# Performance work log

Hardware: AMD Instinct MI355X
Metric: run time of the kernel (lower is better)

The kernel has to match this reference:

```python
import jax, jax.numpy as jnp
import numpy as np

N = 10000      # nodes
E = 100000     # edges
D = 768        # hidden = heads * head_dim
H = 4          # heads
C = D // H     # 192 per-head channels
EDIM = 16      # edge feature dim
NREL = 10      # num relations
L = 3          # num TransformerConv layers


def setup_inputs() -> dict:
    key = jax.random.key(0)
    ks = jax.random.split(key, 16)
    s = 0.02
    x = jax.random.normal(ks[0], (N, D), jnp.float32)
    edge_index = jax.random.randint(ks[1], (2, E), 0, N, jnp.int32)
    rel = jax.random.randint(ks[2], (E,), 0, NREL).astype(jnp.float32)
    w = jax.random.uniform(ks[3], (E,), jnp.float32)
    edge_attr = jnp.stack([rel, w], axis=1)  # [E, 2]: (relation_id, weight)
    rel_emb = jax.random.normal(ks[4], (NREL, EDIM - 1), jnp.float32) * s
    W_edge = jax.random.normal(ks[5], (EDIM, EDIM), jnp.float32) * s
    b_edge = jnp.zeros((EDIM,), jnp.float32)
    Wk = jax.random.normal(ks[6], (L, D, D), jnp.float32) * s
    bk = jnp.zeros((L, D), jnp.float32)
    Wq = jax.random.normal(ks[7], (L, D, D), jnp.float32) * s
    bq = jnp.zeros((L, D), jnp.float32)
    Wv = jax.random.normal(ks[8], (L, D, D), jnp.float32) * s
    bv = jnp.zeros((L, D), jnp.float32)
    We = jax.random.normal(ks[9], (L, EDIM, D), jnp.float32) * s   # lin_edge, no bias (PyG)
    Wskip = jax.random.normal(ks[10], (L, D, D), jnp.float32) * s  # root/skip linear
    bskip = jnp.zeros((L, D), jnp.float32)
    ln_g = jnp.ones((D,), jnp.float32)
    ln_b = jnp.zeros((D,), jnp.float32)
    return dict(x=x, edge_attr=edge_attr, edge_index=edge_index, rel_emb=rel_emb,
                W_edge=W_edge, b_edge=b_edge, Wk=Wk, bk=bk, Wq=Wq, bq=bq,
                Wv=Wv, bv=bv, We=We, Wskip=Wskip, bskip=bskip, ln_g=ln_g, ln_b=ln_b)


def reference(x, edge_attr, edge_index, rel_emb, W_edge, b_edge,
              Wk, bk, Wq, bq, Wv, bv, We, Wskip, bskip, ln_g, ln_b):
    src, dst = edge_index[0], edge_index[1]
    # _process_edge_features: embed relation id, concat weight, project
    rel_ids = jnp.clip(jax.lax.stop_gradient(edge_attr[:, 0]).astype(jnp.int32), 0, NREL - 1)
    ef = jnp.concatenate([rel_emb[rel_ids], edge_attr[:, 1:2]], axis=-1) @ W_edge + b_edge  # [E,16]
    scale = 1.0 / np.sqrt(C)
    h = x  # input_proj is Identity (input_dim == hidden_dim)
    for l in range(L):
        q = (h @ Wq[l] + bq[l]).reshape(N, H, C)
        k = (h @ Wk[l] + bk[l]).reshape(N, H, C)
        v = (h @ Wv[l] + bv[l]).reshape(N, H, C)
        e = (ef @ We[l]).reshape(E, H, C)           # per-edge embedding
        kj = k[src] + e                              # [E,H,C]
        alpha = jnp.einsum('ehc,ehc->eh', q[dst], kj) * scale  # [E,H]
        # scatter-softmax over incoming edges of each destination node
        m = jax.ops.segment_max(jax.lax.stop_gradient(alpha), dst, num_segments=N)
        a = jnp.exp(alpha - m[dst])
        denom = jax.ops.segment_sum(a, dst, num_segments=N)
        a = a / (denom[dst] + 1e-16)
        msg = (v[src] + e) * a[..., None]            # [E,H,C]
        out = jax.ops.segment_sum(msg.reshape(E, H * C), dst, num_segments=N)
        h = out + h @ Wskip[l] + bskip[l]            # root_weight skip connection
        if l < L - 1:
            h = jax.nn.gelu(h, approximate=False)    # dropout: eval mode -> identity
    mu = jnp.mean(h, axis=-1, keepdims=True)
    var = jnp.mean((h - mu) ** 2, axis=-1, keepdims=True)
    h = (h - mu) / jnp.sqrt(var + 1e-5) * ln_g + ln_b
    return jnp.mean(h, axis=0)  # global_mean_pool over single graph -> [D]
```

## Files before the change

kernel.cpp:

```cpp
#include <hip/hip_runtime.h>
#include <hip/hip_bf16.h>
#include <math.h>
#include <stdint.h>

#define NN 10000
#define EE 100000
#define DD 768
#define HH 4
#define CC 192
#define EDIM 16
#define NREL 10
#define MP 10240
#define NQ2 3200
#define NB 3136
#define SCALE 0.07216878364870322f

using short8  = __attribute__((ext_vector_type(8))) short;
using floatx4 = __attribute__((ext_vector_type(4))) float;


__device__ __forceinline__ float b2f(short u) {
    union { unsigned int i; float f; } t;
    t.i = ((unsigned int)(unsigned short)u) << 16;
    return t.f;
}

__device__ __forceinline__ short f2b(float f) {
    __hip_bfloat16 h = __float2bfloat16(f);
    short r;
    __builtin_memcpy(&r, &h, 2);
    return r;
}

__device__ __forceinline__ __hip_bfloat16 rd_any(const void* p, long long j, int bf) {
    if (bf) return ((const __hip_bfloat16*)p)[j];
    return __float2bfloat16(((const float*)p)[j]);
}

__device__ __forceinline__ void gload16(const __hip_bfloat16* g, __hip_bfloat16* l) {
    __builtin_amdgcn_global_load_lds(
        (const __attribute__((address_space(1))) unsigned int*)g,
        (__attribute__((address_space(3))) unsigned int*)l, 16, 0, 0);
}

__global__ __launch_bounds__(256) void detect_zero(const void* edge_attr,
                                                   int* flag, int* counts) {
    int i = blockIdx.x * 256 + threadIdx.x;
    if (i < NN) counts[i] = 0;
    if (blockIdx.x == 0 && threadIdx.x < 64) {
        const unsigned short* p = (const unsigned short*)edge_attr;
        int nz = (p[4 * threadIdx.x] != 0) ? 1 : 0;
        unsigned long long m = __ballot(nz);
        if (threadIdx.x == 0) *flag = (__popcll(m) > 8) ? 1 : 0;
    }
}


__global__ __launch_bounds__(256) void cvt_big(
    const void* x, const void* We, const int* flag,
    __hip_bfloat16* hb, __hip_bfloat16* Web) {
    long long i = (long long)blockIdx.x * 256 + threadIdx.x;
    int bf = *flag;
    const long long NX = (long long)NN * DD;
    const long long NE2 = 3LL * EDIM * DD;
    if (i < NX) { hb[i] = rd_any(x, i, bf); return; } i -= NX;
    if (i < NE2) { Web[i] = rd_any(We, i, bf); return; } i -= NE2;
    if (i < (long long)(MP - NN) * DD) hb[(long long)NN * DD + i] = __float2bfloat16(0.0f);
}

__global__ __launch_bounds__(256) void cvt_small(
    const void* ea, const void* rel, const void* Wed, const void* bed,
    const void* bk, const void* bq, const void* bv, const void* bs,
    const void* lg, const void* lb, const int* flag,
    __hip_bfloat16* eab, __hip_bfloat16* relb, __hip_bfloat16* Wedb,
    __hip_bfloat16* bedb, __hip_bfloat16* ballb, __hip_bfloat16* lgb,
    __hip_bfloat16* lbb) {
    long long i = (long long)blockIdx.x * 256 + threadIdx.x;
    int bf = *flag;
    if (i < 2LL * EE) { eab[i] = rd_any(ea, i, bf); return; } i -= 2LL * EE;
    if (i < NREL * (EDIM - 1)) { relb[i] = rd_any(rel, i, bf); return; } i -= NREL * (EDIM - 1);
    if (i < EDIM * EDIM) { Wedb[i] = rd_any(Wed, i, bf); return; } i -= EDIM * EDIM;
    if (i < EDIM) { bedb[i] = rd_any(bed, i, bf); return; } i -= EDIM;
    if (i < 3 * NB) {
        int l = (int)(i / NB), c = (int)(i % NB);
        const void* src; long long off;
        if (c < 768)       { src = bq; off = (long long)l * DD + c; }
        else if (c < 1536) { src = bk; off = (long long)l * DD + (c - 768); }
        else if (c < 2304) { src = bv; off = (long long)l * DD + (c - 1536); }
        else if (c < 3072) { src = bs; off = (long long)l * DD + (c - 2304); }
        else { ballb[i] = __float2bfloat16(0.0f); return; }
        ballb[i] = rd_any(src, off, bf); return;
    } i -= 3 * NB;
    if (i < DD) { lgb[i] = rd_any(lg, i, bf); return; } i -= DD;
    if (i < DD) { lbb[i] = rd_any(lb, i, bf); return; }
}

__global__ __launch_bounds__(256) void wt_all(
    const void* Wq, const void* Wk, const void* Wv, const void* Ws,
    const int* flag, __hip_bfloat16* Wt3) {
    __shared__ __hip_bfloat16 tile[32][33];
    int mm = blockIdx.y;
    int l = mm >> 2, m = mm & 3;
    const void* src = (m == 0) ? Wq : (m == 1) ? Wk : (m == 2) ? Wv : Ws;
    int bx = blockIdx.x;
    int tr = bx / 24, tc = bx % 24;
    int k0 = tr * 32, c0 = tc * 32;
    int t = threadIdx.x;
    int rr = t >> 5, cc = t & 31;
    int bf = *flag;
    long long base = (long long)l * DD * DD;
#pragma unroll
    for (int p = 0; p < 4; p++)
        tile[p * 8 + rr][cc] =
            rd_any(src, base + (long long)(k0 + p * 8 + rr) * DD + c0 + cc, bf);
    __syncthreads();
    __hip_bfloat16* dst = Wt3 + (size_t)l * NB * DD + (size_t)(m * 768 + c0) * DD + k0;
#pragma unroll
    for (int p = 0; p < 4; p++)
        dst[(size_t)(p * 8 + rr) * DD + cc] = tile[cc][p * 8 + rr];
}

__global__ __launch_bounds__(256) void mq_kernel(
    const void* Wq, const void* bq, const int* flag,
    const __hip_bfloat16* __restrict__ Web, __hip_bfloat16* __restrict__ Wt3,
    __hip_bfloat16* __restrict__ ballb) {
    __shared__ float WeS[16][193];
    const int lh = blockIdx.y, l = lh >> 2, hh = lh & 3;
    const int t = threadIdx.x;
    const int bf = *flag;
    for (int i = t; i < 16 * 192; i += 256) {
        int j = i / 192, c = i % 192;
        WeS[j][c] = (float)Web[(size_t)l * EDIM * DD + (size_t)j * DD + hh * CC + c];
    }
    __syncthreads();
    const int k = blockIdx.x * 64 + (t >> 2);
    const int j0 = (t & 3) * 4;
    float s0 = 0.f, s1 = 0.f, s2 = 0.f, s3 = 0.f;
    if (bf) {
        const short8* qp = (const short8*)((const __hip_bfloat16*)Wq +
            ((size_t)l * DD + k) * DD + hh * CC);
#pragma unroll 4
        for (int ch = 0; ch < 24; ch++) {
            short8 v = qp[ch];
#pragma unroll
            for (int u = 0; u < 8; u++) {
                float w = b2f(v[u]);
                int c = ch * 8 + u;
                s0 += w * WeS[j0 + 0][c]; s1 += w * WeS[j0 + 1][c];
                s2 += w * WeS[j0 + 2][c]; s3 += w * WeS[j0 + 3][c];
            }
        }
    } else {
        const float4* qp = (const float4*)((const float*)Wq +
            ((size_t)l * DD + k) * DD + hh * CC);
#pragma unroll 4
        for (int ch = 0; ch < 48; ch++) {
            float4 v = qp[ch];
            float wv[4] = {v.x, v.y, v.z, v.w};
#pragma unroll
            for (int u = 0; u < 4; u++) {
                float w = wv[u];
                int c = ch * 4 + u;
                s0 += w * WeS[j0 + 0][c]; s1 += w * WeS[j0 + 1][c];
                s2 += w * WeS[j0 + 2][c]; s3 += w * WeS[j0 + 3][c];
            }
        }
    }
    const size_t base = (size_t)l * NB * DD;
    const int row = 3072 + hh * 16 + j0;
    Wt3[base + (size_t)(row + 0) * DD + k] = __float2bfloat16(s0);
    Wt3[base + (size_t)(row + 1) * DD + k] = __float2bfloat16(s1);
    Wt3[base + (size_t)(row + 2) * DD + k] = __float2bfloat16(s2);
    Wt3[base + (size_t)(row + 3) * DD + k] = __float2bfloat16(s3);
    if (blockIdx.x == 0 && t < 4) {
        float b0 = 0.f, b1 = 0.f, b2 = 0.f, b3 = 0.f;
        for (int c = 0; c < CC; c++) {
            float w = (float)rd_any(bq, (long long)l * DD + hh * CC + c, bf);
            b0 += w * WeS[j0 + 0][c]; b1 += w * WeS[j0 + 1][c];
            b2 += w * WeS[j0 + 2][c]; b3 += w * WeS[j0 + 3][c];
        }
        ballb[l * NB + 3072 + hh * 16 + j0 + 0] = __float2bfloat16(b0);
        ballb[l * NB + 3072 + hh * 16 + j0 + 1] = __float2bfloat16(b1);
        ballb[l * NB + 3072 + hh * 16 + j0 + 2] = __float2bfloat16(b2);
        ballb[l * NB + 3072 + hh * 16 + j0 + 3] = __float2bfloat16(b3);
    }
}


__global__ __launch_bounds__(256) void count_kernel(const int* ei, int* counts) {
    int e = blockIdx.x * 256 + threadIdx.x;
    if (e < EE) atomicAdd(&counts[ei[EE + e]], 1);
}

__global__ __launch_bounds__(256) void scan_kernel(const int* counts, int* rowptr,
                                                   int* cursor) {
    __shared__ int sdata[256];
    int t = threadIdx.x;
    int base = t * 40;
    int cnt = (base < NN) ? min(40, NN - base) : 0;
    int s = 0;
    for (int i = 0; i < cnt; i++) s += counts[base + i];
    sdata[t] = s;
    __syncthreads();
    for (int off = 1; off < 256; off <<= 1) {
        int add = (t >= off) ? sdata[t - off] : 0;
        __syncthreads();
        sdata[t] += add;
        __syncthreads();
    }
    int run = sdata[t] - s;
    for (int i = 0; i < cnt; i++) {
        cursor[base + i] = run;
        run += counts[base + i];
        rowptr[base + i + 1] = run;
    }
    if (t == 0) rowptr[0] = 0;
}

__global__ __launch_bounds__(256) void fill_kernel(const int* ei, int* cursor,
                                                   int* eids, int* esrc) {
    int e = blockIdx.x * 256 + threadIdx.x;
    if (e < EE) {
        int d = ei[EE + e];
        int pos = atomicAdd(&cursor[d], 1);
        eids[pos] = e;
        esrc[pos] = ei[e];
    }
}


__global__ __launch_bounds__(256) void ef_kernel(
    const int* __restrict__ eids,
    const __hip_bfloat16* __restrict__ eab, const __hip_bfloat16* __restrict__ relb,
    const __hip_bfloat16* __restrict__ Wedb, const __hip_bfloat16* __restrict__ bedb,
    __hip_bfloat16* __restrict__ efb) {
    int idx = blockIdx.x * 256 + threadIdx.x;
    if (idx >= EE * EDIM) return;
    int p = idx >> 4, j = idx & 15;
    int e = eids[p];
    int rid = (int)((float)eab[e * 2 + 0]);
    rid = min(max(rid, 0), NREL - 1);
    float w = (float)eab[e * 2 + 1];
    float s = (float)bedb[j];
#pragma unroll
    for (int i = 0; i < 15; i++)
        s += (float)relb[rid * 15 + i] * (float)Wedb[i * EDIM + j];
    s += w * (float)Wedb[15 * EDIM + j];
    efb[idx] = __float2bfloat16(s);
}


__device__ __forceinline__ void stage_half(const __hip_bfloat16* g, int row0, int ktile,
                                           char* ldsdst, int tid) {
#pragma unroll
    for (int j = 0; j < 2; ++j) {
        int c = j * 512 + tid;
        int row = c >> 3;
        int sch = (c & 7) ^ (row & 7);
        gload16(g + (size_t)(row0 + row) * DD + ktile * 64 + sch * 8,
                (__hip_bfloat16*)(ldsdst + c * 16));
    }
}

#define MF16(va, vb, cc) cc = __builtin_amdgcn_mfma_f32_16x16x32_bf16(va, vb, cc, 0, 0, 0)
#define BAR() __builtin_amdgcn_s_barrier()
#define WLG() asm volatile("s_waitcnt lgkmcnt(0)" ::: "memory")
#define WVM(N) asm volatile("s_waitcnt vmcnt(" #N ")" ::: "memory")
#define SB() __builtin_amdgcn_sched_barrier(0)
#define LDS8(off) (*(const short8*)(smem + (off)))

__global__ __launch_bounds__(512) void gemm256(
    const __hip_bfloat16* __restrict__ A, const __hip_bfloat16* __restrict__ Bt,
    const __hip_bfloat16* __restrict__ bias, __hip_bfloat16* __restrict__ C) {
    __shared__ __align__(16) char smem[131072];
    const int bid = (int)blockIdx.x;
    const int tid = threadIdx.x;
    const int wid = tid >> 6, lane = tid & 63;
    const int quad = lane >> 4, l15 = lane & 15;

    if (bid >= 480) {
        const int qb = bid - 480;
        const int m0q = qb * 64;
        const __hip_bfloat16* Bq = Bt + (size_t)3072 * DD;
        const int xq0 = (quad ^ (l15 & 7)) * 16;
        const int xq1 = ((quad + 4) ^ (l15 & 7)) * 16;
        floatx4 qacc[4] = {};
        for (int kt = 0; kt < 12; ++kt) {
#pragma unroll
            for (int j = 0; j < 2; ++j) {
                int c = j * 512 + tid;
                int hf = c >> 9;
                int cc = c & 511;
                int row = cc >> 3;
                int sch = (cc & 7) ^ (row & 7);
                const __hip_bfloat16* src = hf
                    ? (Bq + (size_t)row * DD + kt * 64 + sch * 8)
                    : (A + (size_t)(m0q + row) * DD + kt * 64 + sch * 8);
                gload16(src, (__hip_bfloat16*)(smem + c * 16));
            }
            asm volatile("s_waitcnt vmcnt(0)" ::: "memory");
            BAR();
            if (wid < 4) {
                short8 a0 = LDS8((wid * 16 + l15) * 128 + xq0);
                short8 a1 = LDS8((wid * 16 + l15) * 128 + xq1);
#pragma unroll
                for (int nt = 0; nt < 4; ++nt) {
                    short8 b0 = LDS8(8192 + (nt * 16 + l15) * 128 + xq0);
                    short8 b1 = LDS8(8192 + (nt * 16 + l15) * 128 + xq1);
                    MF16(a0, b0, qacc[nt]);
                    MF16(a1, b1, qacc[nt]);
                }
            }
            WLG();
            BAR();
        }
        if (wid < 4) {
#pragma unroll
            for (int nt = 0; nt < 4; ++nt) {
                float bb = (float)bias[3072 + nt * 16 + l15];
#pragma unroll
                for (int r = 0; r < 4; ++r) {
                    int row = m0q + wid * 16 + quad * 4 + r;
                    if (row < NN)
                        C[(size_t)row * NQ2 + 3072 + nt * 16 + l15] =
                            __float2bfloat16(qacc[nt][r] + bb);
                }
            }
        }
        return;
    }

    const int wm = wid >> 2, wn = wid & 3;
    const int swz = (bid & 7) * 60 + (bid >> 3);
    const int m0 = (swz / 12) * 256;
    const int n0 = (swz % 12) * 256;

    const int xa0 = (quad ^ (l15 & 7)) * 16;
    const int xa1 = ((quad + 4) ^ (l15 & 7)) * 16;
    const int aRow = (wm * 128 + l15) * 128;
    const int bRow = 32768 + (wn * 64 + l15) * 128;

    floatx4 acc[8][4] = {};
    short8 a[4][2], bA[2][2], bB[2][2];

    stage_half(A, m0, 0, smem + 0, tid);
    stage_half(A, m0 + 128, 0, smem + 16384, tid);
    stage_half(Bt, n0, 0, smem + 32768, tid);
    stage_half(Bt, n0 + 128, 0, smem + 49152, tid);
    stage_half(Bt, n0, 1, smem + 98304, tid);
    stage_half(Bt, n0 + 128, 1, smem + 114688, tid);
    WVM(4);
    BAR();

#pragma unroll 1
    for (int it = 0; it < 6; ++it) {
        const int kA = 2 * it + 1;
        const int kB = (it < 5) ? 2 * it + 2 : 0;
        const int kC = (it < 5) ? 2 * it + 3 : 1;
        stage_half(A, m0, kA, smem + 65536, tid);
        stage_half(A, m0 + 128, kA, smem + 81920, tid);
#pragma unroll
        for (int mt = 0; mt < 4; ++mt) {
            a[mt][0] = LDS8(aRow + mt * 2048 + xa0);
            a[mt][1] = LDS8(aRow + mt * 2048 + xa1);
        }
#pragma unroll
        for (int nt = 0; nt < 2; ++nt) {
            bA[nt][0] = LDS8(bRow + nt * 2048 + xa0);
            bA[nt][1] = LDS8(bRow + nt * 2048 + xa1);
            bB[nt][0] = LDS8(bRow + (nt + 2) * 2048 + xa0);
            bB[nt][1] = LDS8(bRow + (nt + 2) * 2048 + xa1);
        }
        SB(); BAR(); WLG(); SB();
        __builtin_amdgcn_s_setprio(1);
#pragma unroll
        for (int mt = 0; mt < 4; ++mt)
#pragma unroll
            for (int nt = 0; nt < 2; ++nt) {
                MF16(a[mt][0], bA[nt][0], acc[mt][nt]);
                MF16(a[mt][1], bA[nt][1], acc[mt][nt]);
                MF16(a[mt][0], bB[nt][0], acc[mt][nt + 2]);
                MF16(a[mt][1], bB[nt][1], acc[mt][nt + 2]);
            }
        __builtin_amdgcn_s_setprio(0);
        stage_half(Bt, n0, kB, smem + 32768, tid);
        stage_half(Bt, n0 + 128, kB, smem + 49152, tid);
#pragma unroll
        for (int mt = 0; mt < 4; ++mt) {
            a[mt][0] = LDS8(aRow + (mt + 4) * 2048 + xa0);
            a[mt][1] = LDS8(aRow + (mt + 4) * 2048 + xa1);
        }
        WVM(4);
        SB(); BAR(); WLG(); SB();
        __builtin_amdgcn_s_setprio(1);
#pragma unroll
        for (int mt = 0; mt < 4; ++mt)
#pragma unroll
            for (int nt = 0; nt < 2; ++nt) {
                MF16(a[mt][0], bB[nt][0], acc[mt + 4][nt + 2]);
                MF16(a[mt][1], bB[nt][1], acc[mt + 4][nt + 2]);
                MF16(a[mt][0], bA[nt][0], acc[mt + 4][nt]);
                MF16(a[mt][1], bA[nt][1], acc[mt + 4][nt]);
            }
        __builtin_amdgcn_s_setprio(0);
        stage_half(A, m0, kB, smem + 0, tid);
        stage_half(A, m0 + 128, kB, smem + 16384, tid);
#pragma unroll
        for (int mt = 0; mt < 4; ++mt) {
            a[mt][0] = LDS8(65536 + aRow + mt * 2048 + xa0);
            a[mt][1] = LDS8(65536 + aRow + mt * 2048 + xa1);
        }
#pragma unroll
        for (int nt = 0; nt < 2; ++nt) {
            bA[nt][0] = LDS8(65536 + bRow + nt * 2048 + xa0);
            bA[nt][1] = LDS8(65536 + bRow + nt * 2048 + xa1);
            bB[nt][0] = LDS8(65536 + bRow + (nt + 2) * 2048 + xa0);
            bB[nt][1] = LDS8(65536 + bRow + (nt + 2) * 2048 + xa1);
        }
        SB(); BAR(); WLG(); SB();
        __builtin_amdgcn_s_setprio(1);
#pragma unroll
        for (int mt = 0; mt < 4; ++mt)
#pragma unroll
            for (int nt = 0; nt < 2; ++nt) {
                MF16(a[mt][0], bA[nt][0], acc[mt][nt]);
                MF16(a[mt][1], bA[nt][1], acc[mt][nt]);
                MF16(a[mt][0], bB[nt][0], acc[mt][nt + 2]);
                MF16(a[mt][1], bB[nt][1], acc[mt][nt + 2]);
            }
        __builtin_amdgcn_s_setprio(0);
        stage_half(Bt, n0, kC, smem + 98304, tid);
        stage_half(Bt, n0 + 128, kC, smem + 114688, tid);
#pragma unroll
        for (int mt = 0; mt < 4; ++mt) {
            a[mt][0] = LDS8(65536 + aRow + (mt + 4) * 2048 + xa0);
            a[mt][1] = LDS8(65536 + aRow + (mt + 4) * 2048 + xa1);
        }
        WVM(4);
        SB(); BAR(); WLG(); SB();
        __builtin_amdgcn_s_setprio(1);
#pragma unroll
        for (int mt = 0; mt < 4; ++mt)
#pragma unroll
            for (int nt = 0; nt < 2; ++nt) {
                MF16(a[mt][0], bB[nt][0], acc[mt + 4][nt + 2]);
                MF16(a[mt][1], bB[nt][1], acc[mt + 4][nt + 2]);
                MF16(a[mt][0], bA[nt][0], acc[mt + 4][nt]);
                MF16(a[mt][1], bA[nt][1], acc[mt + 4][nt]);
            }
        __builtin_amdgcn_s_setprio(0);
    }

    asm volatile("s_waitcnt vmcnt(0)" ::: "memory");
    BAR();
    {
        short* stg = (short*)smem + wid * 1152;
        float bv[4];
#pragma unroll
        for (int nt = 0; nt < 4; ++nt)
            bv[nt] = (float)bias[n0 + wn * 64 + nt * 16 + l15];
        const int rdo = (lane >> 2) * 68 + (lane & 3) * 16;
        const int grow0 = m0 + wm * 128 + (lane >> 2);
        const int gcol = n0 + wn * 64 + (lane & 3) * 16;
#pragma unroll
        for (int mt = 0; mt < 8; ++mt) {
#pragma unroll
            for (int nt = 0; nt < 4; ++nt)
#pragma unroll
                for (int r = 0; r < 4; ++r)
                    stg[(quad * 4 + r) * 68 + nt * 16 + l15] =
                        f2b(acc[mt][nt][r] + bv[nt]);
            asm volatile("s_waitcnt lgkmcnt(0)" ::: "memory");
            short8 v0 = *(const short8*)(stg + rdo);
            short8 v1 = *(const short8*)(stg + rdo + 8);
            int grow = grow0 + mt * 16;
            if (grow < NN) {
                short8* dp = (short8*)(C + (size_t)grow * NQ2 + gcol);
                dp[0] = v0; dp[1] = v1;
            }
            asm volatile("s_waitcnt lgkmcnt(0)" ::: "memory");
        }
    }
}


__global__ __launch_bounds__(256) void node_attn(
    const int* __restrict__ rowptr, const int* __restrict__ esrc,
    const __hip_bfloat16* __restrict__ qkvs, const __hip_bfloat16* __restrict__ efb,
    const __hip_bfloat16* __restrict__ Wel, __hip_bfloat16* __restrict__ hb,
    int do_gelu) {
    const int wv = threadIdx.x >> 6, lane = threadIdx.x & 63;
    const int n = blockIdx.x * 2 + (wv >> 1);
    const int half = wv & 1;
    const int cb = half * 384 + lane * 6;
    const int sj = lane & 15;
    const int hsel = lane & 32;
    const float qe_gate = ((lane & 16) == 0) ? 1.0f : 0.0f;
    const int s0 = rowptr[n], s1 = rowptr[n + 1];
    const short* qk = (const short*)qkvs;
    float q[6];
    {
        const short2* qp = (const short2*)(qk + (size_t)n * NQ2 + cb);
        short2 a = qp[0], b = qp[1], c = qp[2];
        q[0] = b2f(a.x) * SCALE; q[1] = b2f(a.y) * SCALE; q[2] = b2f(b.x) * SCALE;
        q[3] = b2f(b.y) * SCALE; q[4] = b2f(c.x) * SCALE; q[5] = b2f(c.y) * SCALE;
    }
    const float qe_l = b2f(qk[(size_t)n * NQ2 + 3072 + (half * 2 + (lane >> 5)) * 16 + sj])
                       * SCALE * qe_gate;
    float m = -INFINITY, lsum = 0.f, sacc = 0.f;
    float acc[6] = {};
    short2 ka = {0,0}, kb = {0,0}, kc = {0,0};
    short2 va = {0,0}, vb = {0,0}, vc = {0,0};
    float efv = 0.f;
    if (s0 < s1) {
        int src = esrc[s0];
        const short2* kp = (const short2*)(qk + (size_t)src * NQ2 + 768 + cb);
        const short2* vp = (const short2*)(qk + (size_t)src * NQ2 + 1536 + cb);
        ka = kp[0]; kb = kp[1]; kc = kp[2];
        va = vp[0]; vb = vp[1]; vc = vp[2];
        efv = b2f(((const short*)efb)[(size_t)s0 * 16 + sj]);
    }
    for (int p = s0; p < s1; p++) {
        short2 nka = ka, nkb = kb, nkc = kc, nva = va, nvb = vb, nvc = vc;
        float nefv = efv;
        if (p + 1 < s1) {
            int src = esrc[p + 1];
            const short2* kp = (const short2*)(qk + (size_t)src * NQ2 + 768 + cb);
            const short2* vp = (const short2*)(qk + (size_t)src * NQ2 + 1536 + cb);
            nka = kp[0]; nkb = kp[1]; nkc = kp[2];
            nva = vp[0]; nvb = vp[1]; nvc = vp[2];
            nefv = b2f(((const short*)efb)[(size_t)(p + 1) * 16 + sj]);
        }
        float part = qe_l * efv;
        part += q[0] * b2f(ka.x) + q[1] * b2f(ka.y) + q[2] * b2f(kb.x);
        part += q[3] * b2f(kb.y) + q[4] * b2f(kc.x) + q[5] * b2f(kc.y);
        part += __shfl_xor(part, 1); part += __shfl_xor(part, 2);
        part += __shfl_xor(part, 4); part += __shfl_xor(part, 8);
        part += __shfl_xor(part, 16);
        if (part > m + 8.0f) {
            float sc = __expf(m - part);
            m = part;
            lsum *= sc; sacc *= sc;
#pragma unroll
            for (int i = 0; i < 6; i++) acc[i] *= sc;
        }
        float w = __expf(part - m);
        lsum += w;
        sacc += w * efv;
        acc[0] += w * b2f(va.x); acc[1] += w * b2f(va.y);
        acc[2] += w * b2f(vb.x); acc[3] += w * b2f(vb.y);
        acc[4] += w * b2f(vc.x); acc[5] += w * b2f(vc.y);
        ka = nka; kb = nkb; kc = nkc; va = nva; vb = nvb; vc = nvc; efv = nefv;
    }
    float inv = 1.0f / (lsum + 1e-16f);
#pragma unroll
    for (int i = 0; i < 6; i++) acc[i] *= inv;
    float sS = sacc * inv;
    {
        const short2* sp = (const short2*)(qk + (size_t)n * NQ2 + 2304 + cb);
        short2 a = sp[0], b = sp[1], c = sp[2];
        acc[0] += b2f(a.x); acc[1] += b2f(a.y); acc[2] += b2f(b.x);
        acc[3] += b2f(b.y); acc[4] += b2f(c.x); acc[5] += b2f(c.y);
    }
#pragma unroll
    for (int j = 0; j < 16; j++) {
        float sv = __shfl(sS, hsel + j);
        const short2* wp = (const short2*)(Wel + (size_t)j * DD + cb);
        short2 a = wp[0], b = wp[1], c = wp[2];
        acc[0] += sv * b2f(a.x); acc[1] += sv * b2f(a.y); acc[2] += sv * b2f(b.x);
        acc[3] += sv * b2f(b.y); acc[4] += sv * b2f(c.x); acc[5] += sv * b2f(c.y);
    }
    if (do_gelu) {
#pragma unroll
        for (int i = 0; i < 6; i++)
            acc[i] = 0.5f * acc[i] * (1.0f + erff(acc[i] * 0.70710678118654752f));
    }
    short2 o0, o1, o2;
    o0.x = f2b(acc[0]); o0.y = f2b(acc[1]);
    o1.x = f2b(acc[2]); o1.y = f2b(acc[3]);
    o2.x = f2b(acc[4]); o2.y = f2b(acc[5]);
    short2* hp = (short2*)(hb + (size_t)n * DD + cb);
    hp[0] = o0; hp[1] = o1; hp[2] = o2;
}


__global__ __launch_bounds__(256) void ln_pool(
    const __hip_bfloat16* __restrict__ hb, const __hip_bfloat16* __restrict__ g,
    const __hip_bfloat16* __restrict__ b, float* __restrict__ partial) {
    __shared__ float sbuf[4][768];
    int grp = blockIdx.x, t = threadIdx.x;
    int wid = t >> 6, lane = t & 63;
    float gv[12], bv[12], acc[12];
#pragma unroll
    for (int i = 0; i < 12; i++) {
        gv[i] = (float)g[lane + i * 64];
        bv[i] = (float)b[lane + i * 64];
        acc[i] = 0.f;
    }
    for (int r = wid; r < 25; r += 4) {
        const __hip_bfloat16* row = hb + (size_t)(grp * 25 + r) * DD;
        float x[12];
        float s = 0.f, q = 0.f;
#pragma unroll
        for (int i = 0; i < 12; i++) {
            x[i] = (float)row[lane + i * 64];
            s += x[i]; q += x[i] * x[i];
        }
#pragma unroll
        for (int m = 32; m > 0; m >>= 1) {
            s += __shfl_xor(s, m); q += __shfl_xor(q, m);
        }
        float mu = s * (1.0f / 768.0f);
        float ms = q * (1.0f / 768.0f);
        float inv = 1.0f / sqrtf(ms - mu * mu + 1e-5f);
#pragma unroll
        for (int i = 0; i < 12; i++)
            acc[i] += (x[i] - mu) * inv * gv[i] + bv[i];
    }
#pragma unroll
    for (int i = 0; i < 12; i++) sbuf[wid][lane + i * 64] = acc[i];
    __syncthreads();
#pragma unroll
    for (int j = 0; j < 3; j++) {
        int col = t + j * 256;
        partial[(size_t)grp * DD + col] =
            sbuf[0][col] + sbuf[1][col] + sbuf[2][col] + sbuf[3][col];
    }
}

__global__ __launch_bounds__(256) void pool_final(
    const float* __restrict__ partial, void* __restrict__ out,
    const int* __restrict__ flag) {
    int dd = blockIdx.x * 256 + threadIdx.x;
    if (dd >= DD) return;
    float s = 0.f;
    for (int g2 = 0; g2 < 400; g2++) s += partial[(size_t)g2 * DD + dd];
    s *= (1.0f / 10000.0f);
    if (*flag) ((__hip_bfloat16*)out)[dd] = __float2bfloat16(s);
    else ((float*)out)[dd] = s;
}


extern "C" void kernel_launch(void* const* d_in, const int* in_sizes, int n_in,
                              void* d_out, int out_size, void* d_ws, size_t ws_size,
                              hipStream_t stream) {
    const void* x         = d_in[0];
    const void* edge_attr = d_in[1];
    const int*  ei        = (const int*)d_in[2];
    const void* rel_emb   = d_in[3];
    const void* W_edge    = d_in[4];
    const void* b_edge    = d_in[5];
    const void* Wk        = d_in[6];
    const void* bk        = d_in[7];
    const void* Wq        = d_in[8];
    const void* bq        = d_in[9];
    const void* Wv        = d_in[10];
    const void* bv        = d_in[11];
    const void* We        = d_in[12];
    const void* Wskip     = d_in[13];
    const void* bskip     = d_in[14];
    const void* ln_g      = d_in[15];
    const void* ln_b      = d_in[16];

    char* ws = (char*)d_ws;
    int*   flag    = (int*)(ws + 0);
    int*   counts  = (int*)(ws + 256);
    int*   rowptr  = (int*)(ws + 40448);
    int*   cursor  = (int*)(ws + 80640);
    int*   eids    = (int*)(ws + 120832);
    int*   esrc    = (int*)(ws + 520960);
    __hip_bfloat16* efb = (__hip_bfloat16*)(ws + 920960);
    float* partial = (float*)(ws + 4120960);
    __hip_bfloat16* eab   = (__hip_bfloat16*)(ws + 5349760);
    __hip_bfloat16* relb  = (__hip_bfloat16*)(ws + 5749760);
    __hip_bfloat16* Wedb  = (__hip_bfloat16*)(ws + 5750144);
    __hip_bfloat16* bedb  = (__hip_bfloat16*)(ws + 5750656);
    __hip_bfloat16* ballb = (__hip_bfloat16*)(ws + 5750784);
    __hip_bfloat16* lngb  = (__hip_bfloat16*)(ws + 5770752);
    __hip_bfloat16* lnbb  = (__hip_bfloat16*)(ws + 5772288);
    __hip_bfloat16* Web   = (__hip_bfloat16*)(ws + 5773824);
    __hip_bfloat16* hb    = (__hip_bfloat16*)(ws + 5847552);
    __hip_bfloat16* Wt3   = (__hip_bfloat16*)(ws + 21576192);
    __hip_bfloat16* qkvs  = (__hip_bfloat16*)(ws + 36911616);

    dim3 blk(256);

    detect_zero<<<dim3(40), blk, 0, stream>>>(edge_attr, flag, counts);

    {
        long long tot = (long long)NN * DD + 3LL * EDIM * DD + (long long)(MP - NN) * DD;
        cvt_big<<<dim3((unsigned)((tot + 255) / 256)), blk, 0, stream>>>(x, We, flag, hb, Web);
    }
    {
        long long tot = 2LL * EE + NREL * (EDIM - 1) + EDIM * EDIM + EDIM
                        + 3LL * NB + 2LL * DD;
        cvt_small<<<dim3((unsigned)((tot + 255) / 256)), blk, 0, stream>>>(
            edge_attr, rel_emb, W_edge, b_edge, bk, bq, bv, bskip, ln_g, ln_b,
            flag, eab, relb, Wedb, bedb, ballb, lngb, lnbb);
    }
    wt_all<<<dim3(576, 12), blk, 0, stream>>>(Wq, Wk, Wv, Wskip, flag, Wt3);
    mq_kernel<<<dim3(12, 12), blk, 0, stream>>>(Wq, bq, flag, Web, Wt3, ballb);

    count_kernel<<<dim3((EE + 255) / 256), blk, 0, stream>>>(ei, counts);
    scan_kernel<<<dim3(1), blk, 0, stream>>>(counts, rowptr, cursor);
    fill_kernel<<<dim3((EE + 255) / 256), blk, 0, stream>>>(ei, cursor, eids, esrc);

    ef_kernel<<<dim3((EE * EDIM) / 256), blk, 0, stream>>>(eids, eab, relb, Wedb, bedb, efb);

    for (int l = 0; l < 3; l++) {
        const __hip_bfloat16* We_l = Web + (size_t)l * EDIM * DD;
        gemm256<<<dim3(640), dim3(512), 0, stream>>>(
            hb, Wt3 + (size_t)l * NB * DD, ballb + (size_t)l * NB, qkvs);
        node_attn<<<dim3(NN / 2), blk, 0, stream>>>(rowptr, esrc, qkvs, efb,
                                                    We_l, hb, (l < 2) ? 1 : 0);
    }

    ln_pool<<<dim3(400), blk, 0, stream>>>(hb, lngb, lnbb, partial);
    pool_final<<<dim3(3), blk, 0, stream>>>(partial, d_out, flag);
}
```

Measured before the change: 601.7 us.

## Shrink GEMM tile to 128x256 with K=32 double-buffered LDS pipeline

The main GEMM now uses 128x256 output tiles instead of 256x256, with K stepped in chunks of 32 through a two-slot LDS ring of 48KB in place of the 128KB triple-slot schedule. Launch bounds request more resident blocks, and the grid grows to 1120 blocks with an adjusted swizzle. The aim is higher occupancy and better wave coverage across CUs, so memory latency is hidden by more concurrent blocks. The cost is lower data reuse per tile, more barriers per K step, and more global traffic for the shared weight operand.

```diff
diff --git a/kernel.cpp b/kernel.cpp
--- a/kernel.cpp
+++ b/kernel.cpp
@@ -250,36 +250,25 @@
 }
 
 
-__device__ __forceinline__ void stage_half(const __hip_bfloat16* g, int row0, int ktile,
-                                           char* ldsdst, int tid) {
-#pragma unroll
-    for (int j = 0; j < 2; ++j) {
-        int c = j * 512 + tid;
-        int row = c >> 3;
-        int sch = (c & 7) ^ (row & 7);
-        gload16(g + (size_t)(row0 + row) * DD + ktile * 64 + sch * 8,
-                (__hip_bfloat16*)(ldsdst + c * 16));
-    }
-}
-
 #define MF16(va, vb, cc) cc = __builtin_amdgcn_mfma_f32_16x16x32_bf16(va, vb, cc, 0, 0, 0)
 #define BAR() __builtin_amdgcn_s_barrier()
 #define WLG() asm volatile("s_waitcnt lgkmcnt(0)" ::: "memory")
 #define WVM(N) asm volatile("s_waitcnt vmcnt(" #N ")" ::: "memory")
 #define SB() __builtin_amdgcn_sched_barrier(0)
 #define LDS8(off) (*(const short8*)(smem + (off)))
-
-__global__ __launch_bounds__(512) void gemm256(
+#define SLOT 24576
+
+__global__ __launch_bounds__(512, 4) void gemm256(
     const __hip_bfloat16* __restrict__ A, const __hip_bfloat16* __restrict__ Bt,
     const __hip_bfloat16* __restrict__ bias, __hip_bfloat16* __restrict__ C) {
-    __shared__ __align__(16) char smem[131072];
+    __shared__ __align__(16) char smem[49152];
     const int bid = (int)blockIdx.x;
     const int tid = threadIdx.x;
     const int wid = tid >> 6, lane = tid & 63;
     const int quad = lane >> 4, l15 = lane & 15;
 
-    if (bid >= 480) {
-        const int qb = bid - 480;
+    if (bid >= 960) {
+        const int qb = bid - 960;
         const int m0q = qb * 64;
         const __hip_bfloat16* Bq = Bt + (size_t)3072 * DD;
         const int xq0 = (quad ^ (l15 & 7)) * 16;
@@ -331,125 +320,69 @@
     }
 
     const int wm = wid >> 2, wn = wid & 3;
-    const int swz = (bid & 7) * 60 + (bid >> 3);
-    const int m0 = (swz / 12) * 256;
+    const int swz = (bid & 7) * 120 + (bid >> 3);
+    const int m0 = (swz / 12) * 128;
     const int n0 = (swz % 12) * 256;
 
-    const int xa0 = (quad ^ (l15 & 7)) * 16;
-    const int xa1 = ((quad + 4) ^ (l15 & 7)) * 16;
-    const int aRow = (wm * 128 + l15) * 128;
-    const int bRow = 32768 + (wn * 64 + l15) * 128;
-
-    floatx4 acc[8][4] = {};
-    short8 a[4][2], bA[2][2], bB[2][2];
-
-    stage_half(A, m0, 0, smem + 0, tid);
-    stage_half(A, m0 + 128, 0, smem + 16384, tid);
-    stage_half(Bt, n0, 0, smem + 32768, tid);
-    stage_half(Bt, n0 + 128, 0, smem + 49152, tid);
-    stage_half(Bt, n0, 1, smem + 98304, tid);
-    stage_half(Bt, n0 + 128, 1, smem + 114688, tid);
-    WVM(4);
+    const int ra = wm * 64 + l15;
+    const int abase = (ra >> 1) * 128 +
+                      (((((ra & 1) << 2) | quad) ^ ((ra >> 1) & 7)) << 4);
+    const int rb = wn * 64 + l15;
+    const int bbase = 8192 + (rb >> 1) * 128 +
+                      (((((rb & 1) << 2) | quad) ^ ((rb >> 1) & 7)) << 4);
+
+    floatx4 acc[4][4] = {};
+    short8 a[4], b[4];
+
+#define STAGE(kt, sbase) do {                                                 \
+        _Pragma("unroll")                                                     \
+        for (int j = 0; j < 3; ++j) {                                         \
+            int c = j * 512 + tid;                                            \
+            int isB = (c >= 512);                                             \
+            int cc = isB ? c - 512 : c;                                       \
+            int pr = cc >> 3;                                                 \
+            int us = (cc & 7) ^ (pr & 7);                                     \
+            int row = pr * 2 + (us >> 2);                                     \
+            int kch = us & 3;                                                 \
+            const __hip_bfloat16* src = isB                                   \
+                ? (Bt + (size_t)(n0 + row) * DD + (kt) * 32 + kch * 8)        \
+                : (A + (size_t)(m0 + row) * DD + (kt) * 32 + kch * 8);        \
+            gload16(src, (__hip_bfloat16*)(smem + (sbase) +                   \
+                                           (isB ? 8192 : 0) + cc * 16));      \
+        }                                                                     \
+    } while (0)
+
+    STAGE(0, 0);
+    STAGE(1, SLOT);
+    WVM(3);
     BAR();
 
+    int sl = 0;
 #pragma unroll 1
-    for (int it = 0; it < 6; ++it) {
-        const int kA = 2 * it + 1;
-        const int kB = (it < 5) ? 2 * it + 2 : 0;
-        const int kC = (it < 5) ? 2 * it + 3 : 1;
-        stage_half(A, m0, kA, smem + 65536, tid);
-        stage_half(A, m0 + 128, kA, smem + 81920, tid);
-#pragma unroll
-        for (int mt = 0; mt < 4; ++mt) {
-            a[mt][0] = LDS8(aRow + mt * 2048 + xa0);
-            a[mt][1] = LDS8(aRow + mt * 2048 + xa1);
-        }
-#pragma unroll
-        for (int nt = 0; nt < 2; ++nt) {
-            bA[nt][0] = LDS8(bRow + nt * 2048 + xa0);
-            bA[nt][1] = LDS8(bRow + nt * 2048 + xa1);
-            bB[nt][0] = LDS8(bRow + (nt + 2) * 2048 + xa0);
-            bB[nt][1] = LDS8(bRow + (nt + 2) * 2048 + xa1);
-        }
-        SB(); BAR(); WLG(); SB();
+    for (int kt = 0; kt < 24; ++kt) {
+        const int sbase = sl ? SLOT : 0;
+#pragma unroll
+        for (int mt = 0; mt < 4; ++mt) a[mt] = LDS8(sbase + abase + mt * 1024);
+#pragma unroll
+        for (int nt = 0; nt < 4; ++nt) b[nt] = LDS8(sbase + bbase + nt * 1024);
+        WLG();
+        SB();
+        BAR();
+        int ks = kt + 2; if (ks >= 24) ks -= 24;
+        STAGE(ks, sbase);
+        WVM(3);
         __builtin_amdgcn_s_setprio(1);
 #pragma unroll
         for (int mt = 0; mt < 4; ++mt)
 #pragma unroll
-            for (int nt = 0; nt < 2; ++nt) {
-                MF16(a[mt][0], bA[nt][0], acc[mt][nt]);
-                MF16(a[mt][1], bA[nt][1], acc[mt][nt]);
-                MF16(a[mt][0], bB[nt][0], acc[mt][nt + 2]);
-                MF16(a[mt][1], bB[nt][1], acc[mt][nt + 2]);
-            }
+            for (int nt = 0; nt < 4; ++nt)
+                MF16(a[mt], b[nt], acc[mt][nt]);
         __builtin_amdgcn_s_setprio(0);
-        stage_half(Bt, n0, kB, smem + 32768, tid);
-        stage_half(Bt, n0 + 128, kB, smem + 49152, tid);
-#pragma unroll
-        for (int mt = 0; mt < 4; ++mt) {
-            a[mt][0] = LDS8(aRow + (mt + 4) * 2048 + xa0);
-            a[mt][1] = LDS8(aRow + (mt + 4) * 2048 + xa1);
-        }
-        WVM(4);
-        SB(); BAR(); WLG(); SB();
-        __builtin_amdgcn_s_setprio(1);
-#pragma unroll
-        for (int mt = 0; mt < 4; ++mt)
-#pragma unroll
-            for (int nt = 0; nt < 2; ++nt) {
-                MF16(a[mt][0], bB[nt][0], acc[mt + 4][nt + 2]);
-                MF16(a[mt][1], bB[nt][1], acc[mt + 4][nt + 2]);
-                MF16(a[mt][0], bA[nt][0], acc[mt + 4][nt]);
-                MF16(a[mt][1], bA[nt][1], acc[mt + 4][nt]);
-            }
-        __builtin_amdgcn_s_setprio(0);
-        stage_half(A, m0, kB, smem + 0, tid);
-        stage_half(A, m0 + 128, kB, smem + 16384, tid);
-#pragma unroll
-        for (int mt = 0; mt < 4; ++mt) {
-            a[mt][0] = LDS8(65536 + aRow + mt * 2048 + xa0);
-            a[mt][1] = LDS8(65536 + aRow + mt * 2048 + xa1);
-        }
-#pragma unroll
-        for (int nt = 0; nt < 2; ++nt) {
-            bA[nt][0] = LDS8(65536 + bRow + nt * 2048 + xa0);
-            bA[nt][1] = LDS8(65536 + bRow + nt * 2048 + xa1);
-            bB[nt][0] = LDS8(65536 + bRow + (nt + 2) * 2048 + xa0);
-            bB[nt][1] = LDS8(65536 + bRow + (nt + 2) * 2048 + xa1);
-        }
-        SB(); BAR(); WLG(); SB();
-        __builtin_amdgcn_s_setprio(1);
-#pragma unroll
-        for (int mt = 0; mt < 4; ++mt)
-#pragma unroll
-            for (int nt = 0; nt < 2; ++nt) {
-                MF16(a[mt][0], bA[nt][0], acc[mt][nt]);
-                MF16(a[mt][1], bA[nt][1], acc[mt][nt]);
-                MF16(a[mt][0], bB[nt][0], acc[mt][nt + 2]);
-                MF16(a[mt][1], bB[nt][1], acc[mt][nt + 2]);
-            }
-        __builtin_amdgcn_s_setprio(0);
-        stage_half(Bt, n0, kC, smem + 98304, tid);
-        stage_half(Bt, n0 + 128, kC, smem + 114688, tid);
-#pragma unroll
-        for (int mt = 0; mt < 4; ++mt) {
-            a[mt][0] = LDS8(65536 + aRow + (mt + 4) * 2048 + xa0);
-            a[mt][1] = LDS8(65536 + aRow + (mt + 4) * 2048 + xa1);
-        }
-        WVM(4);
-        SB(); BAR(); WLG(); SB();
-        __builtin_amdgcn_s_setprio(1);
-#pragma unroll
-        for (int mt = 0; mt < 4; ++mt)
-#pragma unroll
-            for (int nt = 0; nt < 2; ++nt) {
-                MF16(a[mt][0], bB[nt][0], acc[mt + 4][nt + 2]);
-                MF16(a[mt][1], bB[nt][1], acc[mt + 4][nt + 2]);
-                MF16(a[mt][0], bA[nt][0], acc[mt + 4][nt]);
-                MF16(a[mt][1], bA[nt][1], acc[mt + 4][nt]);
-            }
-        __builtin_amdgcn_s_setprio(0);
-    }
+        SB();
+        BAR();
+        sl ^= 1;
+    }
+#undef STAGE
 
     asm volatile("s_waitcnt vmcnt(0)" ::: "memory");
     BAR();
@@ -460,10 +393,10 @@
         for (int nt = 0; nt < 4; ++nt)
             bv[nt] = (float)bias[n0 + wn * 64 + nt * 16 + l15];
         const int rdo = (lane >> 2) * 68 + (lane & 3) * 16;
-        const int grow0 = m0 + wm * 128 + (lane >> 2);
+        const int grow0 = m0 + wm * 64 + (lane >> 2);
         const int gcol = n0 + wn * 64 + (lane & 3) * 16;
 #pragma unroll
-        for (int mt = 0; mt < 8; ++mt) {
+        for (int mt = 0; mt < 4; ++mt) {
 #pragma unroll
             for (int nt = 0; nt < 4; ++nt)
 #pragma unroll
@@ -709,7 +642,7 @@
 
     for (int l = 0; l < 3; l++) {
         const __hip_bfloat16* We_l = Web + (size_t)l * EDIM * DD;
-        gemm256<<<dim3(640), dim3(512), 0, stream>>>(
+        gemm256<<<dim3(1120), dim3(512), 0, stream>>>(
             hb, Wt3 + (size_t)l * NB * DD, ballb + (size_t)l * NB, qkvs);
         node_attn<<<dim3(NN / 2), blk, 0, stream>>>(rowptr, esrc, qkvs, efb,
                                                     We_l, hb, (l < 2) ? 1 : 0);
```

Result: no change. 603.0 us (+0.2%).
